# Optimization experiments

Hardware: AMD Instinct MI355X
Metric: run time of the kernel (lower is better)

Reference implementation:

```python
import jax, jax.numpy as jnp
import numpy as np
import math

EPS = 1.1920929e-07  # torch.finfo(float32).eps, used by nn.RMSNorm when eps=None
N_HEADS = 16

def _rmsnorm(x, w):
    return x * jax.lax.rsqrt(jnp.mean(x * x, axis=-1, keepdims=True) + EPS) * w

def setup_inputs() -> dict:
    key = jax.random.key(0)
    D, V, FF = 1024, 32000, 2048
    NS, IPS = 4, 8
    B, T = 2, 1024
    ks = jax.random.split(key, 8)
    sd = 0.02
    g = lambda i, shape: jax.random.normal(ks[i], shape, jnp.float32) * sd
    return {
        "tokens": jax.random.randint(ks[0], (B, T), 0, V),
        "embed_w": g(1, (V, D)),
        "qkv_w": g(2, (3 * D, D)),
        "o_w": g(3, (D, D)),
        "gate_w": g(4, (FF, D)),
        "up_w": g(5, (FF, D)),
        "down_w": g(6, (D, FF)),
        "norm1_w": jnp.ones((D,), jnp.float32),
        "norm2_w": jnp.ones((D,), jnp.float32),
        "scale_gamma": jnp.ones((NS, D), jnp.float32),
        "scale_beta": jnp.zeros((NS, D), jnp.float32),
        "iter_scale": jnp.ones((NS, IPS), jnp.float32),
        "norm_w": jnp.ones((D,), jnp.float32),
        "lm_head_w": g(7, (V, D)),
    }

def _block(x, gamma, beta, qkv_w, o_w, gate_w, up_w, down_w, norm1_w, norm2_w):
    B, T, D = x.shape
    hd = D // N_HEADS
    # pre-attn norm + FiLM modulation
    h = _rmsnorm(x, norm1_w) * gamma + beta
    qkv = (h @ qkv_w.T).reshape(B, T, 3, N_HEADS, hd)
    q = jnp.transpose(qkv[:, :, 0], (0, 2, 1, 3))  # [B,H,T,hd]
    k = jnp.transpose(qkv[:, :, 1], (0, 2, 1, 3))
    v = jnp.transpose(qkv[:, :, 2], (0, 2, 1, 3))
    scores = jnp.einsum('bhqd,bhkd->bhqk', q, k) / math.sqrt(hd)
    causal = jnp.tril(jnp.ones((T, T), dtype=bool))
    scores = jnp.where(causal, scores, -jnp.inf)
    attn = jax.nn.softmax(scores, axis=-1)
    out = jnp.einsum('bhqk,bhkd->bhqd', attn, v)
    out = jnp.transpose(out, (0, 2, 1, 3)).reshape(B, T, D)
    x = x + out @ o_w.T
    # pre-FFN norm + FiLM modulation, SwiGLU
    h2 = _rmsnorm(x, norm2_w) * gamma + beta
    x = x + (jax.nn.silu(h2 @ gate_w.T) * (h2 @ up_w.T)) @ down_w.T
    return x

def reference(tokens, embed_w, qkv_w, o_w, gate_w, up_w, down_w, norm1_w,
              norm2_w, scale_gamma, scale_beta, iter_scale, norm_w, lm_head_w):
    NS, IPS = iter_scale.shape
    x = embed_w[tokens].astype(jnp.float32)  # [B,T,D]
    # flatten (scale, iter) schedule to per-virtual-layer params [NS*IPS, ...]
    gammas = jnp.repeat(scale_gamma, IPS, axis=0)
    betas = jnp.repeat(scale_beta, IPS, axis=0)
    iters = iter_scale.reshape(-1)

    @jax.checkpoint
    def step(x, per):
        g, b, s = per
        y = _block(x, g, b, qkv_w, o_w, gate_w, up_w, down_w, norm1_w, norm2_w)
        return x + (y - x) * s, None

    x, _ = jax.lax.scan(step, x, (gammas, betas, iters))
    return _rmsnorm(x, norm_w) @ lm_head_w.T  # [B,T,V]
```

## Files before the change

kernel.cpp:

```cpp
#include <hip/hip_runtime.h>

typedef __bf16 bf16;
typedef __attribute__((ext_vector_type(8))) __bf16 bf16x8;
typedef __attribute__((ext_vector_type(4))) __bf16 bf16x4;
typedef __attribute__((ext_vector_type(4))) float f32x4;

#define MFMA16(a,b,c) __builtin_amdgcn_mfma_f32_16x16x32_bf16((a),(b),(c),0,0,0)

__device__ __forceinline__ void gload16(const void* g, void* l) {
    __builtin_amdgcn_global_load_lds((const __attribute__((address_space(1))) void*)g,
                                     (__attribute__((address_space(3))) void*)l, 16, 0, 0);
}

__device__ __forceinline__ int xcd_swizzle(int orig, int nwg) {
    int q = nwg >> 3, r = nwg & 7;
    int xcd = orig & 7, loc = orig >> 3;
    int base = (xcd < r) ? xcd * (q + 1) : r * (q + 1) + (xcd - r) * q;
    return base + loc;
}


__global__ __launch_bounds__(256) void cvt_kernel(const float* __restrict__ in,
                                                  bf16* __restrict__ out, int n4) {
    int stride = gridDim.x * 256;
    for (int i = blockIdx.x * 256 + threadIdx.x; i < n4; i += stride) {
        float4 v = ((const float4*)in)[i];
        bf16x4 o;
        o[0] = (bf16)v.x; o[1] = (bf16)v.y; o[2] = (bf16)v.z; o[3] = (bf16)v.w;
        ((bf16x4*)out)[i] = o;
    }
}

__global__ __launch_bounds__(256) void embed_kernel(const int* __restrict__ tok,
                                                    const float* __restrict__ ew,
                                                    float* __restrict__ X) {
    int m = blockIdx.x;
    int t = tok[m];
    ((float4*)(X + (size_t)m * 1024))[threadIdx.x] =
        ((const float4*)(ew + (size_t)t * 1024))[threadIdx.x];
}

template <bool FILM>
__global__ __launch_bounds__(256) void rmsnorm_kernel(const float* __restrict__ X,
                                                      const float* __restrict__ w,
                                                      const float* __restrict__ gamma,
                                                      const float* __restrict__ beta,
                                                      bf16* __restrict__ H) {
    int m = blockIdx.x, t = threadIdx.x;
    float4 xv = ((const float4*)(X + (size_t)m * 1024))[t];
    float ss = xv.x * xv.x + xv.y * xv.y + xv.z * xv.z + xv.w * xv.w;
#pragma unroll
    for (int off = 1; off < 64; off <<= 1) ss += __shfl_xor(ss, off);
    __shared__ float red[4];
    if ((t & 63) == 0) red[t >> 6] = ss;
    __syncthreads();
    float tot = red[0] + red[1] + red[2] + red[3];
    float sc = rsqrtf(tot * (1.0f / 1024.0f) + 1.1920929e-07f);
    float4 wv = ((const float4*)w)[t];
    float r0 = xv.x * sc * wv.x, r1 = xv.y * sc * wv.y;
    float r2 = xv.z * sc * wv.z, r3 = xv.w * sc * wv.w;
    if (FILM) {
        float4 gv = ((const float4*)gamma)[t];
        float4 bv = ((const float4*)beta)[t];
        r0 = r0 * gv.x + bv.x; r1 = r1 * gv.y + bv.y;
        r2 = r2 * gv.z + bv.z; r3 = r3 * gv.w + bv.w;
    }
    bf16x4 o;
    o[0] = (bf16)r0; o[1] = (bf16)r1; o[2] = (bf16)r2; o[3] = (bf16)r3;
    ((bf16x4*)(H + (size_t)m * 1024))[t] = o;
}


template <int MT, int MODE, bool BNF>
__global__ __launch_bounds__(256, 2) void gemm_bt(const bf16* __restrict__ A,
                                                  const bf16* __restrict__ B,
                                                  int GN, int GM,
                                                  int N, int K,
                                                  bf16* __restrict__ Cb, float* __restrict__ Cf,
                                                  const float* __restrict__ Xin,
                                                  const float* __restrict__ Xin2,
                                                  float* __restrict__ Xout,
                                                  const float* __restrict__ sptr) {
    constexpr int BM = 32 * MT;
    __shared__ __align__(16) bf16 As[BM * 64];
    __shared__ __align__(16) bf16 Bs[128 * 64];
    const int wg = xcd_swizzle(blockIdx.x, GN * GM);
    int bn, bm;
    if (BNF) { bm = wg / GN; bn = wg - bm * GN; }
    else     { bn = wg / GM; bm = wg - bn * GM; }
    const int tid = threadIdx.x, lane = tid & 63, w = tid >> 6;
    const int wr = w >> 1, wc = w & 1, lr = lane & 15, lg = lane >> 4;
    const bf16* Ab = A + (size_t)bm * BM * K;
    const bf16* Bb = B + (size_t)bn * 128 * K;

    f32x4 acc[MT][4];
#pragma unroll
    for (int i = 0; i < MT; ++i)
#pragma unroll
        for (int j = 0; j < 4; ++j) acc[i][j] = (f32x4){0.f, 0.f, 0.f, 0.f};

    for (int kt = 0; kt < K; kt += 64) {
        __syncthreads();
#pragma unroll
        for (int i = 0; i < MT; ++i) {
            int cw = i * 256 + w * 64;
            int cid = cw + lane;
            gload16(Ab + (size_t)(cid >> 3) * K + kt + (cid & 7) * 8, As + cw * 8);
        }
#pragma unroll
        for (int i = 0; i < 4; ++i) {
            int cw = i * 256 + w * 64;
            int cid = cw + lane;
            gload16(Bb + (size_t)(cid >> 3) * K + kt + (cid & 7) * 8, Bs + cw * 8);
        }
        __syncthreads();
#pragma unroll
        for (int kk = 0; kk < 64; kk += 32) {
            bf16x8 af[MT], bfr[4];
#pragma unroll
            for (int mi = 0; mi < MT; ++mi)
                af[mi] = *(const bf16x8*)(As + (wr * (16 * MT) + mi * 16 + lr) * 64 + kk + lg * 8);
#pragma unroll
            for (int ni = 0; ni < 4; ++ni)
                bfr[ni] = *(const bf16x8*)(Bs + (wc * 64 + ni * 16 + lr) * 64 + kk + lg * 8);
#pragma unroll
            for (int mi = 0; mi < MT; ++mi)
#pragma unroll
                for (int ni = 0; ni < 4; ++ni)
                    acc[mi][ni] = MFMA16(af[mi], bfr[ni], acc[mi][ni]);
        }
    }

    float s1 = (MODE == 2) ? sptr[0] : 0.f;
#pragma unroll
    for (int mi = 0; mi < MT; ++mi) {
#pragma unroll
        for (int ni = 0; ni < 4; ++ni) {
#pragma unroll
            for (int j = 0; j < 4; ++j) {
                int row = bm * BM + wr * (16 * MT) + mi * 16 + lg * 4 + j;
                int col = bn * 128 + wc * 64 + ni * 16 + lr;
                size_t idx = (size_t)row * N + col;
                float v = acc[mi][ni][j];
                if (MODE == 0) Cb[idx] = (bf16)v;
                else if (MODE == 1) Xout[idx] = Xin[idx] + v;
                else if (MODE == 2) Xout[idx] = Xin[idx] + s1 * (Xin2[idx] - Xin[idx] + v);
                else Cf[idx] = v;
            }
        }
    }
}


__global__ __launch_bounds__(256, 2) void gemm_gateup(const bf16* __restrict__ A,
                                                      const bf16* __restrict__ Bg,
                                                      const bf16* __restrict__ Bu,
                                                      bf16* __restrict__ FF) {
    const int K = 1024, N = 2048;
    __shared__ __align__(16) bf16 As[128 * 64];
    __shared__ __align__(16) bf16 Gs[128 * 64];
    __shared__ __align__(16) bf16 Us[128 * 64];
    const int wg = xcd_swizzle(blockIdx.x, 256);
    const int bn = wg >> 4, bm = wg & 15;
    const int tid = threadIdx.x, lane = tid & 63, w = tid >> 6;
    const int wr = w >> 1, wc = w & 1, lr = lane & 15, lg = lane >> 4;
    const bf16* Ab = A + (size_t)bm * 128 * K;
    const bf16* Gb = Bg + (size_t)bn * 128 * K;
    const bf16* Ub = Bu + (size_t)bn * 128 * K;

    f32x4 ag[4][4], au[4][4];
#pragma unroll
    for (int i = 0; i < 4; ++i)
#pragma unroll
        for (int j = 0; j < 4; ++j) {
            ag[i][j] = (f32x4){0.f, 0.f, 0.f, 0.f};
            au[i][j] = (f32x4){0.f, 0.f, 0.f, 0.f};
        }

    for (int kt = 0; kt < K; kt += 64) {
        __syncthreads();
#pragma unroll
        for (int i = 0; i < 4; ++i) {
            int cw = i * 256 + w * 64;
            int cid = cw + lane;
            size_t ro = (size_t)(cid >> 3) * K + kt + (cid & 7) * 8;
            gload16(Ab + ro, As + cw * 8);
            gload16(Gb + ro, Gs + cw * 8);
            gload16(Ub + ro, Us + cw * 8);
        }
        __syncthreads();
#pragma unroll
        for (int kk = 0; kk < 64; kk += 32) {
            bf16x8 af[4], gf[4], uf[4];
#pragma unroll
            for (int mi = 0; mi < 4; ++mi)
                af[mi] = *(const bf16x8*)(As + (wr * 64 + mi * 16 + lr) * 64 + kk + lg * 8);
#pragma unroll
            for (int ni = 0; ni < 4; ++ni) {
                gf[ni] = *(const bf16x8*)(Gs + (wc * 64 + ni * 16 + lr) * 64 + kk + lg * 8);
                uf[ni] = *(const bf16x8*)(Us + (wc * 64 + ni * 16 + lr) * 64 + kk + lg * 8);
            }
#pragma unroll
            for (int mi = 0; mi < 4; ++mi)
#pragma unroll
                for (int ni = 0; ni < 4; ++ni) {
                    ag[mi][ni] = MFMA16(af[mi], gf[ni], ag[mi][ni]);
                    au[mi][ni] = MFMA16(af[mi], uf[ni], au[mi][ni]);
                }
        }
    }

#pragma unroll
    for (int mi = 0; mi < 4; ++mi) {
#pragma unroll
        for (int ni = 0; ni < 4; ++ni) {
#pragma unroll
            for (int j = 0; j < 4; ++j) {
                int row = bm * 128 + wr * 64 + mi * 16 + lg * 4 + j;
                int col = bn * 128 + wc * 64 + ni * 16 + lr;
                float g = ag[mi][ni][j], u = au[mi][ni][j];
                float sg = g / (1.0f + __expf(-g));
                FF[(size_t)row * N + col] = (bf16)(sg * u);
            }
        }
    }
}


__global__ __launch_bounds__(256) void attn_kernel(const bf16* __restrict__ QKV,
                                                   bf16* __restrict__ AO) {
    const int qt = blockIdx.x, bh = blockIdx.y;
    const int b = bh >> 4, h = bh & 15;
    const int tid = threadIdx.x;
    const int w = tid >> 6, lane = tid & 63;
    const int lr = lane & 15, lg = lane >> 4;

    __shared__ __align__(16) bf16 Ks[64 * 72];
    __shared__ __align__(16) bf16 Vt[64 * 72];
    __shared__ __align__(16) bf16 Ps[4 * 16 * 72];
    bf16* Pw = Ps + w * 16 * 72;

    const int qrow = b * 1024 + qt * 64 + w * 16 + lr;
    const bf16* qptr = QKV + (size_t)qrow * 3072 + h * 64;
    bf16x8 qf0 = *(const bf16x8*)(qptr + lg * 8);
    bf16x8 qf1 = *(const bf16x8*)(qptr + 32 + lg * 8);

    f32x4 o[4];
#pragma unroll
    for (int i = 0; i < 4; ++i) o[i] = (f32x4){0.f, 0.f, 0.f, 0.f};
    float m_run = -1e30f, l_run = 0.f;
    const int gq = qt * 64 + w * 16 + lr;

    for (int kt = 0; kt <= qt; ++kt) {
        __syncthreads();
#pragma unroll
        for (int i = 0; i < 2; ++i) {
            int cid = tid + 256 * i;
            int r = cid >> 3, c8 = (cid & 7) * 8;
            const bf16* kvrow = QKV + (size_t)(b * 1024 + kt * 64 + r) * 3072 + h * 64;
            *(bf16x8*)(Ks + r * 72 + c8) = *(const bf16x8*)(kvrow + 1024 + c8);
            bf16x8 vv = *(const bf16x8*)(kvrow + 2048 + c8);
#pragma unroll
            for (int ii = 0; ii < 8; ++ii) Vt[(c8 + ii) * 72 + r] = vv[ii];
        }
        __syncthreads();

        f32x4 st[4];
#pragma unroll
        for (int i = 0; i < 4; ++i) st[i] = (f32x4){0.f, 0.f, 0.f, 0.f};
        __builtin_amdgcn_s_setprio(1);
#pragma unroll
        for (int ki = 0; ki < 4; ++ki) {
            bf16x8 kf0 = *(const bf16x8*)(Ks + (ki * 16 + lr) * 72 + lg * 8);
            bf16x8 kf1 = *(const bf16x8*)(Ks + (ki * 16 + lr) * 72 + 32 + lg * 8);
            st[ki] = MFMA16(kf0, qf0, st[ki]);
            st[ki] = MFMA16(kf1, qf1, st[ki]);
        }
        __builtin_amdgcn_s_setprio(0);
        bool diag = (kt == qt);
        float pm = -1e30f;
#pragma unroll
        for (int ki = 0; ki < 4; ++ki) {
#pragma unroll
            for (int j = 0; j < 4; ++j) {
                float sv = st[ki][j] * 0.125f;
                if (diag) {
                    int gk = kt * 64 + ki * 16 + lg * 4 + j;
                    if (gk > gq) sv = -1e30f;
                }
                st[ki][j] = sv;
                pm = fmaxf(pm, sv);
            }
        }
        pm = fmaxf(pm, __shfl_xor(pm, 16));
        pm = fmaxf(pm, __shfl_xor(pm, 32));
        float m_new = fmaxf(m_run, pm);
        float alpha = __expf(m_run - m_new);
        float rs = 0.f;
#pragma unroll
        for (int ki = 0; ki < 4; ++ki) {
            bf16x4 pb;
#pragma unroll
            for (int j = 0; j < 4; ++j) {
                float pv = __expf(st[ki][j] - m_new);
                rs += pv;
                pb[j] = (bf16)pv;
            }
            *(bf16x4*)(Pw + lr * 72 + ki * 16 + lg * 4) = pb;
        }
        rs += __shfl_xor(rs, 16);
        rs += __shfl_xor(rs, 32);
        l_run = l_run * alpha + rs;
        m_run = m_new;
#pragma unroll
        for (int di = 0; di < 4; ++di) o[di] *= alpha;
        __builtin_amdgcn_s_setprio(1);
#pragma unroll
        for (int dk = 0; dk < 2; ++dk) {
            bf16x8 pf = *(const bf16x8*)(Pw + lr * 72 + dk * 32 + lg * 8);
#pragma unroll
            for (int di = 0; di < 4; ++di) {
                bf16x8 vf = *(const bf16x8*)(Vt + (di * 16 + lr) * 72 + dk * 32 + lg * 8);
                o[di] = MFMA16(vf, pf, o[di]);
            }
        }
        __builtin_amdgcn_s_setprio(0);
    }
    float inv = 1.0f / l_run;
    bf16* optr = AO + (size_t)qrow * 1024 + h * 64;
#pragma unroll
    for (int di = 0; di < 4; ++di) {
        bf16x4 ov;
#pragma unroll
        for (int j = 0; j < 4; ++j) ov[j] = (bf16)(o[di][j] * inv);
        *(bf16x4*)(optr + di * 16 + lg * 4) = ov;
    }
}


extern "C" void kernel_launch(void* const* d_in, const int* in_sizes, int n_in,
                              void* d_out, int out_size, void* d_ws, size_t ws_size,
                              hipStream_t stream) {
    const int* tokens = (const int*)d_in[0];
    const float* embed_w = (const float*)d_in[1];
    const float* qkv_w = (const float*)d_in[2];
    const float* o_w = (const float*)d_in[3];
    const float* gate_w = (const float*)d_in[4];
    const float* up_w = (const float*)d_in[5];
    const float* down_w = (const float*)d_in[6];
    const float* norm1_w = (const float*)d_in[7];
    const float* norm2_w = (const float*)d_in[8];
    const float* scale_gamma = (const float*)d_in[9];
    const float* scale_beta = (const float*)d_in[10];
    const float* iter_scale = (const float*)d_in[11];
    const float* norm_w = (const float*)d_in[12];
    const float* lm_head_w = (const float*)d_in[13];

    char* p = (char*)d_ws;
    auto alloc = [&](size_t nbytes) -> char* {
        char* r = p;
        p += (nbytes + 255) & ~(size_t)255;
        return r;
    };
    bf16* WQKV = (bf16*)alloc(3072ull * 1024 * 2);
    bf16* WO   = (bf16*)alloc(1024ull * 1024 * 2);
    bf16* WG   = (bf16*)alloc(2048ull * 1024 * 2);
    bf16* WU   = (bf16*)alloc(2048ull * 1024 * 2);
    bf16* WD   = (bf16*)alloc(1024ull * 2048 * 2);
    bf16* WLM  = (bf16*)alloc(32000ull * 1024 * 2);
    float* X   = (float*)alloc(2048ull * 1024 * 4);
    float* X1  = (float*)alloc(2048ull * 1024 * 4);
    bf16* H    = (bf16*)alloc(2048ull * 1024 * 2);
    bf16* QKVb = (bf16*)alloc(2048ull * 3072 * 2);
    bf16* AO   = (bf16*)alloc(2048ull * 1024 * 2);
    bf16* FF   = (bf16*)alloc(2048ull * 2048 * 2);

    cvt_kernel<<<1024, 256, 0, stream>>>(qkv_w, WQKV, 3072 * 1024 / 4);
    cvt_kernel<<<1024, 256, 0, stream>>>(o_w, WO, 1024 * 1024 / 4);
    cvt_kernel<<<1024, 256, 0, stream>>>(gate_w, WG, 2048 * 1024 / 4);
    cvt_kernel<<<1024, 256, 0, stream>>>(up_w, WU, 2048 * 1024 / 4);
    cvt_kernel<<<1024, 256, 0, stream>>>(down_w, WD, 1024 * 2048 / 4);
    cvt_kernel<<<2048, 256, 0, stream>>>(lm_head_w, WLM, 32000 * 1024 / 4);
    embed_kernel<<<2048, 256, 0, stream>>>(tokens, embed_w, X);

    for (int l = 0; l < 32; ++l) {
        const float* gm = scale_gamma + (size_t)(l >> 3) * 1024;
        const float* bt = scale_beta + (size_t)(l >> 3) * 1024;
        rmsnorm_kernel<true><<<2048, 256, 0, stream>>>(X, norm1_w, gm, bt, H);
        gemm_bt<4, 0, false><<<24 * 16, 256, 0, stream>>>(H, WQKV, 24, 16, 3072, 1024,
                                                          QKVb, nullptr, nullptr, nullptr, nullptr, nullptr);
        attn_kernel<<<dim3(16, 32), 256, 0, stream>>>(QKVb, AO);
        gemm_bt<2, 1, true><<<8 * 32, 256, 0, stream>>>(AO, WO, 8, 32, 1024, 1024,
                                                        nullptr, nullptr, X, nullptr, X1, nullptr);
        rmsnorm_kernel<true><<<2048, 256, 0, stream>>>(X1, norm2_w, gm, bt, H);
        gemm_gateup<<<256, 256, 0, stream>>>(H, WG, WU, FF);
        gemm_bt<2, 2, true><<<8 * 32, 256, 0, stream>>>(FF, WD, 8, 32, 1024, 2048,
                                                        nullptr, nullptr, X, X1, X, iter_scale + l);
    }
    rmsnorm_kernel<false><<<2048, 256, 0, stream>>>(X, norm_w, nullptr, nullptr, H);
    gemm_bt<4, 3, false><<<250 * 16, 256, 0, stream>>>(H, WLM, 250, 16, 32000, 1024,
                                                       nullptr, (float*)d_out, nullptr, nullptr, nullptr, nullptr);
}
```

Baseline: 5.282 ms.

## Write V transposed from QKV GEMM epilogue and load it directly in attention

The QKV GEMM gets a new epilogue mode: tiles in the V column range are written into a per-head transposed buffer [b,h,d,t] instead of the row-major QKV buffer. The attention kernel then loads V^T tiles with vectorized 16-byte copies instead of scalar scattered LDS stores, which removes the per-element transpose on every key tile. The cost is 8-byte strided global stores in the GEMM epilogue, plus a workspace buffer.

```diff
diff --git a/kernel.cpp b/kernel.cpp
--- a/kernel.cpp
+++ b/kernel.cpp
@@ -80,7 +80,8 @@
                                                   const float* __restrict__ Xin,
                                                   const float* __restrict__ Xin2,
                                                   float* __restrict__ Xout,
-                                                  const float* __restrict__ sptr) {
+                                                  const float* __restrict__ sptr,
+                                                  bf16* __restrict__ VTp) {
     constexpr int BM = 32 * MT;
     __shared__ __align__(16) bf16 As[BM * 64];
     __shared__ __align__(16) bf16 Bs[128 * 64];
@@ -132,6 +133,23 @@
     }
 
     float s1 = (MODE == 2) ? sptr[0] : 0.f;
+    if (MODE == 4 && bn >= 16) {
+#pragma unroll
+        for (int mi = 0; mi < MT; ++mi) {
+#pragma unroll
+            for (int ni = 0; ni < 4; ++ni) {
+                int row0 = bm * BM + wr * (16 * MT) + mi * 16 + lg * 4;
+                int col = bn * 128 + wc * 64 + ni * 16 + lr;
+                int h = (col - 2048) >> 6, d = (col - 2048) & 63;
+                int bb = row0 >> 10, t0 = row0 & 1023;
+                bf16x4 pv;
+#pragma unroll
+                for (int j = 0; j < 4; ++j) pv[j] = (bf16)acc[mi][ni][j];
+                *(bf16x4*)(VTp + (size_t)(bb * 16 + h) * 65536 + (size_t)d * 1024 + t0) = pv;
+            }
+        }
+        return;
+    }
 #pragma unroll
     for (int mi = 0; mi < MT; ++mi) {
 #pragma unroll
@@ -142,7 +160,7 @@
                 int col = bn * 128 + wc * 64 + ni * 16 + lr;
                 size_t idx = (size_t)row * N + col;
                 float v = acc[mi][ni][j];
-                if (MODE == 0) Cb[idx] = (bf16)v;
+                if (MODE == 0 || MODE == 4) Cb[idx] = (bf16)v;
                 else if (MODE == 1) Xout[idx] = Xin[idx] + v;
                 else if (MODE == 2) Xout[idx] = Xin[idx] + s1 * (Xin2[idx] - Xin[idx] + v);
                 else Cf[idx] = v;
@@ -228,6 +246,7 @@
 
 
 __global__ __launch_bounds__(256) void attn_kernel(const bf16* __restrict__ QKV,
+                                                   const bf16* __restrict__ VTg,
                                                    bf16* __restrict__ AO) {
     const int qt = blockIdx.x, bh = blockIdx.y;
     const int b = bh >> 4, h = bh & 15;
@@ -242,6 +261,7 @@
 
     const int qrow = b * 1024 + qt * 64 + w * 16 + lr;
     const bf16* qptr = QKV + (size_t)qrow * 3072 + h * 64;
+    const bf16* vt_src = VTg + (size_t)bh * 65536;
     bf16x8 qf0 = *(const bf16x8*)(qptr + lg * 8);
     bf16x8 qf1 = *(const bf16x8*)(qptr + 32 + lg * 8);
 
@@ -259,9 +279,8 @@
             int r = cid >> 3, c8 = (cid & 7) * 8;
             const bf16* kvrow = QKV + (size_t)(b * 1024 + kt * 64 + r) * 3072 + h * 64;
             *(bf16x8*)(Ks + r * 72 + c8) = *(const bf16x8*)(kvrow + 1024 + c8);
-            bf16x8 vv = *(const bf16x8*)(kvrow + 2048 + c8);
-#pragma unroll
-            for (int ii = 0; ii < 8; ++ii) Vt[(c8 + ii) * 72 + r] = vv[ii];
+            *(bf16x8*)(Vt + r * 72 + c8) =
+                *(const bf16x8*)(vt_src + (size_t)r * 1024 + kt * 64 + c8);
         }
         __syncthreads();
 
@@ -372,6 +391,7 @@
     float* X1  = (float*)alloc(2048ull * 1024 * 4);
     bf16* H    = (bf16*)alloc(2048ull * 1024 * 2);
     bf16* QKVb = (bf16*)alloc(2048ull * 3072 * 2);
+    bf16* VT   = (bf16*)alloc(2048ull * 1024 * 2);
     bf16* AO   = (bf16*)alloc(2048ull * 1024 * 2);
     bf16* FF   = (bf16*)alloc(2048ull * 2048 * 2);
 
@@ -387,17 +407,17 @@
         const float* gm = scale_gamma + (size_t)(l >> 3) * 1024;
         const float* bt = scale_beta + (size_t)(l >> 3) * 1024;
         rmsnorm_kernel<true><<<2048, 256, 0, stream>>>(X, norm1_w, gm, bt, H);
-        gemm_bt<4, 0, false><<<24 * 16, 256, 0, stream>>>(H, WQKV, 24, 16, 3072, 1024,
-                                                          QKVb, nullptr, nullptr, nullptr, nullptr, nullptr);
-        attn_kernel<<<dim3(16, 32), 256, 0, stream>>>(QKVb, AO);
+        gemm_bt<4, 4, false><<<24 * 16, 256, 0, stream>>>(H, WQKV, 24, 16, 3072, 1024,
+                                                          QKVb, nullptr, nullptr, nullptr, nullptr, nullptr, VT);
+        attn_kernel<<<dim3(16, 32), 256, 0, stream>>>(QKVb, VT, AO);
         gemm_bt<2, 1, true><<<8 * 32, 256, 0, stream>>>(AO, WO, 8, 32, 1024, 1024,
-                                                        nullptr, nullptr, X, nullptr, X1, nullptr);
+                                                        nullptr, nullptr, X, nullptr, X1, nullptr, nullptr);
         rmsnorm_kernel<true><<<2048, 256, 0, stream>>>(X1, norm2_w, gm, bt, H);
         gemm_gateup<<<256, 256, 0, stream>>>(H, WG, WU, FF);
         gemm_bt<2, 2, true><<<8 * 32, 256, 0, stream>>>(FF, WD, 8, 32, 1024, 2048,
-                                                        nullptr, nullptr, X, X1, X, iter_scale + l);
+                                                        nullptr, nullptr, X, X1, X, iter_scale + l, nullptr);
     }
     rmsnorm_kernel<false><<<2048, 256, 0, stream>>>(X, norm_w, nullptr, nullptr, H);
     gemm_bt<4, 3, false><<<250 * 16, 256, 0, stream>>>(H, WLM, 250, 16, 32000, 1024,
-                                                       nullptr, (float*)d_out, nullptr, nullptr, nullptr, nullptr);
-}
+                                                       nullptr, (float*)d_out, nullptr, nullptr, nullptr, nullptr, nullptr);
+}
```

New measurement: 5.000 ms. 1.06x faster.
